# Kernel tuning notes

Hardware: AMD Instinct MI355X
Metric: run time of the kernel (lower is better)

## Reference

```python
import jax, jax.numpy as jnp
import numpy as np

N, IN_DIM, OUT_DIM = 8192, 256, 128
NEG_BIG = -9e15


def setup_inputs() -> dict:
    key = jax.random.key(0)
    k_x, k_a, k_w, k_att = jax.random.split(key, 4)
    X = jax.random.normal(k_x, (N, IN_DIM), dtype=jnp.float32)
    A = jax.random.randint(k_a, (N, N), 0, 2).astype(jnp.float32)
    # nn.Linear(in_dim, out_dim, bias=False): weight [out_dim, in_dim]
    W = jax.random.normal(k_w, (OUT_DIM, IN_DIM), dtype=jnp.float32) / np.sqrt(IN_DIM)
    # nn.Linear(out_dim, 1, bias=False): weight [1, out_dim] -> store as [out_dim]
    a_w = jax.random.normal(k_att, (OUT_DIM,), dtype=jnp.float32) / np.sqrt(OUT_DIM)
    return {"X": X, "A": A, "W": W, "a_w": a_w}


def reference(X, A, W, a_w):
    Wh = X @ W.T                                  # [N, out_dim]
    e = jax.nn.relu(Wh) @ a_w                      # [N]  (a(relu(Wh)).squeeze(-1))
    # NOTE: faithful to source: e broadcasts over rows -> score[i, j] = e[j]
    scores = jnp.where(A > 0, e[None, :], NEG_BIG)  # [N, N]
    attention = jax.nn.softmax(scores, axis=1)      # [N, N]
    h_prime = attention @ Wh                        # [N, out_dim]
    return jax.nn.relu(h_prime)
```

## Files before the change

### kernel.cpp

```cpp
#include <hip/hip_runtime.h>

typedef float        f32x4  __attribute__((ext_vector_type(4)));
typedef __bf16       bf16x8 __attribute__((ext_vector_type(8)));
typedef unsigned int u32x4  __attribute__((ext_vector_type(4)));

#define NN   8192
#define IND  256
#define OUTD 128
#define NB   144
#define KSPLIT 16
#define KRANGE 512
#define BT_BYTES (144 * 1024)

__device__ __forceinline__ bf16x8 cvt2(f32x4 a, f32x4 b) {
  bf16x8 r;
  r[0]=(__bf16)a[0]; r[1]=(__bf16)a[1]; r[2]=(__bf16)a[2]; r[3]=(__bf16)a[3];
  r[4]=(__bf16)b[0]; r[5]=(__bf16)b[1]; r[6]=(__bf16)b[2]; r[7]=(__bf16)b[3];
  return r;
}

__global__ __launch_bounds__(256) void k1_bt(const float* __restrict__ X,
                                             const float* __restrict__ W,
                                             const float* __restrict__ aw,
                                             __bf16* __restrict__ Bt) {
  __shared__ float red[4][16][128];
  const int tid  = threadIdx.x;
  const int lane = tid & 63;
  const int wave = tid >> 6;
  const int nlo  = lane & 15;
  const int quad = lane >> 4;
  const int rowBase = blockIdx.x * 16;

  const float* xp = X + (size_t)(rowBase + nlo) * IND + wave * 64 + quad * 8;
  f32x4 acc[8];
#pragma unroll
  for (int nt = 0; nt < 8; ++nt) acc[nt] = f32x4{0.f, 0.f, 0.f, 0.f};

#pragma unroll
  for (int kb = 0; kb < 64; kb += 32) {
    f32x4 a0 = *(const f32x4*)(xp + kb);
    f32x4 a1 = *(const f32x4*)(xp + kb + 4);
    bf16x8 af = cvt2(a0, a1);
#pragma unroll
    for (int nt = 0; nt < 8; ++nt) {
      const float* wp = W + (size_t)(nt * 16 + nlo) * IND + wave * 64 + kb + quad * 8;
      f32x4 b0 = *(const f32x4*)wp;
      f32x4 b1 = *(const f32x4*)(wp + 4);
      acc[nt] = __builtin_amdgcn_mfma_f32_16x16x32_bf16(af, cvt2(b0, b1), acc[nt], 0, 0, 0);
    }
  }
#pragma unroll
  for (int nt = 0; nt < 8; ++nt)
#pragma unroll
    for (int rg = 0; rg < 4; ++rg)
      red[wave][quad * 4 + rg][nt * 16 + nlo] = acc[nt][rg];
  __syncthreads();

  const int r  = tid >> 4;
  const int c0 = (tid & 15) * 8;
  f32x4 vlo = *(const f32x4*)&red[0][r][c0];
  f32x4 vhi = *(const f32x4*)&red[0][r][c0 + 4];
#pragma unroll
  for (int w = 1; w < 4; ++w) {
    vlo += *(const f32x4*)&red[w][r][c0];
    vhi += *(const f32x4*)&red[w][r][c0 + 4];
  }
  float pa = 0.f;
#pragma unroll
  for (int i = 0; i < 4; ++i) {
    pa += fmaxf(vlo[i], 0.f) * aw[c0 + i];
    pa += fmaxf(vhi[i], 0.f) * aw[c0 + 4 + i];
  }
#pragma unroll
  for (int off = 8; off; off >>= 1) pa += __shfl_xor(pa, off, 64);
  const float wexp = expf(pa);
  const int j = rowBase + r;

#pragma unroll
  for (int i = 0; i < 4; ++i)
    Bt[(size_t)(c0 + i) * NN + j] = (__bf16)(vlo[i] * wexp);
#pragma unroll
  for (int i = 0; i < 4; ++i)
    Bt[(size_t)(c0 + 4 + i) * NN + j] = (__bf16)(vhi[i] * wexp);
  if ((tid & 15) == 0)
    Bt[(size_t)OUTD * NN + j] = (__bf16)wexp;
  if (tid < 120) {
    const int row = 129 + (tid >> 3);
    const int cc  = rowBase + (tid & 7) * 2;
    Bt[(size_t)row * NN + cc]     = (__bf16)0.f;
    Bt[(size_t)row * NN + cc + 1] = (__bf16)0.f;
  }
}

__global__ __launch_bounds__(512) void k3_partial(const float* __restrict__ Adj,
                                                  const __bf16* __restrict__ Bt,
                                                  float* __restrict__ part) {
  extern __shared__ char btile[];
  const int tid  = threadIdx.x;
  const int lane = tid & 63;
  const int wv   = tid >> 6;
  const int nlo  = lane & 15;
  const int quad = lane >> 4;
  const int rowW = blockIdx.x * 128 + wv * 16;
  const int k0   = blockIdx.y * KRANGE;

  const float* ap = Adj + (size_t)(rowW + nlo) * NN + k0 + quad * 8;

  f32x4 aA[8], aB[8];
#pragma unroll
  for (int s4 = 0; s4 < 4; ++s4) {
    aA[2 * s4]     = __builtin_nontemporal_load((const f32x4*)(ap + s4 * 32));
    aA[2 * s4 + 1] = __builtin_nontemporal_load((const f32x4*)(ap + s4 * 32 + 4));
  }

#pragma unroll
  for (int it = 0; it < 18; ++it) {
    const int row = it * 8 + wv;
    const int swz = (row & 7) << 4;
    u32x4 v = *(const u32x4*)((const char*)(Bt + (size_t)row * NN + k0) + lane * 16);
    *(u32x4*)(btile + row * 1024 + ((lane * 16) ^ swz)) = v;
  }
  __syncthreads();

  f32x4 acc[9];
#pragma unroll
  for (int nt = 0; nt < 9; ++nt) acc[nt] = f32x4{0.f, 0.f, 0.f, 0.f};

  const int swzr = (nlo & 7) << 4;
  for (int c = 0; c < 4; ++c) {
    if (c < 3) {
      const int kc1 = (c + 1) * 128;
#pragma unroll
      for (int s4 = 0; s4 < 4; ++s4) {
        aB[2 * s4]     = __builtin_nontemporal_load((const f32x4*)(ap + kc1 + s4 * 32));
        aB[2 * s4 + 1] = __builtin_nontemporal_load((const f32x4*)(ap + kc1 + s4 * 32 + 4));
      }
    }
#pragma unroll
    for (int s4 = 0; s4 < 4; ++s4) {
      const int s = c * 4 + s4;
      bf16x8 af = cvt2(aA[2 * s4], aA[2 * s4 + 1]);
      const int cbl = s * 64 + quad * 16;
#pragma unroll
      for (int nt = 0; nt < 9; ++nt) {
        bf16x8 bf = *(const bf16x8*)(btile + (nt * 16 + nlo) * 1024 + (cbl ^ swzr));
        acc[nt] = __builtin_amdgcn_mfma_f32_16x16x32_bf16(af, bf, acc[nt], 0, 0, 0);
      }
    }
    if (c < 3) {
#pragma unroll
      for (int s = 0; s < 8; ++s) aA[s] = aB[s];
    }
  }

  float* pbase = part + ((size_t)blockIdx.y * NN + rowW) * NB;
#pragma unroll
  for (int nt = 0; nt < 8; ++nt)
#pragma unroll
    for (int rg = 0; rg < 4; ++rg)
      pbase[(size_t)(quad * 4 + rg) * NB + nt * 16 + nlo] = acc[nt][rg];
  if (nlo == 0) {
#pragma unroll
    for (int rg = 0; rg < 4; ++rg)
      pbase[(size_t)(quad * 4 + rg) * NB + 128] = acc[8][rg];
  }
}

__global__ __launch_bounds__(256) void k3_reduce(const float* __restrict__ part,
                                                 float* __restrict__ out) {
  const int col = threadIdx.x & 127;
  const int row = blockIdx.x * 2 + (threadIdx.x >> 7);
  float num = 0.f, den = 0.f;
#pragma unroll
  for (int s = 0; s < KSPLIT; ++s) {
    const size_t base = ((size_t)s * NN + row) * NB;
    num += part[base + col];
    den += part[base + 128];
  }
  out[(size_t)row * OUTD + col] = fmaxf(num / den, 0.f);
}

extern "C" void kernel_launch(void* const* d_in, const int* in_sizes, int n_in,
                              void* d_out, int out_size, void* d_ws, size_t ws_size,
                              hipStream_t stream) {
  const float* X  = (const float*)d_in[0];
  const float* A  = (const float*)d_in[1];
  const float* W  = (const float*)d_in[2];
  const float* aw = (const float*)d_in[3];
  float* out = (float*)d_out;

  char* ws = (char*)d_ws;
  __bf16* Bt   = (__bf16*)ws;
  float*  part = (float*)(ws + 4194304);

  static bool attr_done = false;
  if (!attr_done) {
    hipFuncSetAttribute((const void*)k3_partial,
                        hipFuncAttributeMaxDynamicSharedMemorySize, BT_BYTES);
    attr_done = true;
  }

  k1_bt<<<512, 256, 0, stream>>>(X, W, aw, Bt);
  k3_partial<<<dim3(64, KSPLIT), 512, BT_BYTES, stream>>>(A, Bt, part);
  k3_reduce<<<4096, 256, 0, stream>>>(part, out);
}
```

Baseline: 423.9 us.

## Stream Bt through small chunked LDS tiles to raise occupancy in k3_partial

The partial aggregation kernel used to stage a whole 144 KB Bt slice in dynamic LDS, which allowed only one 512-thread block per CU. It now loads Bt in 64-column chunks into a padded 20 KB static LDS tile, with a sync per chunk. It uses 256-thread blocks with a 4-block launch bound and halves KSPLIT to 8, giving 1024-wide K ranges. The aim is more resident waves to hide the latency of streaming the adjacency matrix. The cost is that the explicit A double-buffer prefetch is dropped, each chunk needs two barriers, and Bt is re-read from L2 by more row blocks.

```diff
diff --git a/kernel.cpp b/kernel.cpp
--- a/kernel.cpp
+++ b/kernel.cpp
@@ -2,15 +2,16 @@
 
 typedef float        f32x4  __attribute__((ext_vector_type(4)));
 typedef __bf16       bf16x8 __attribute__((ext_vector_type(8)));
-typedef unsigned int u32x4  __attribute__((ext_vector_type(4)));
+typedef unsigned int u32x2  __attribute__((ext_vector_type(2)));
 
 #define NN   8192
 #define IND  256
 #define OUTD 128
 #define NB   144
-#define KSPLIT 16
-#define KRANGE 512
-#define BT_BYTES (144 * 1024)
+#define KSPLIT 8
+#define KRANGE 1024
+#define KCHUNK 64
+#define BSTRIDE 72
 
 __device__ __forceinline__ bf16x8 cvt2(f32x4 a, f32x4 b) {
   bf16x8 r;
@@ -92,65 +93,55 @@
   }
 }
 
-__global__ __launch_bounds__(512) void k3_partial(const float* __restrict__ Adj,
-                                                  const __bf16* __restrict__ Bt,
-                                                  float* __restrict__ part) {
-  extern __shared__ char btile[];
+__global__ __launch_bounds__(256, 4) void k3_partial(const float* __restrict__ Adj,
+                                                     const __bf16* __restrict__ Bt,
+                                                     float* __restrict__ part) {
+  __shared__ unsigned short bt[NB * BSTRIDE];
   const int tid  = threadIdx.x;
   const int lane = tid & 63;
-  const int wv   = tid >> 6;
+  const int wave = tid >> 6;
   const int nlo  = lane & 15;
   const int quad = lane >> 4;
-  const int rowW = blockIdx.x * 128 + wv * 16;
+  const int rowW = blockIdx.x * 64 + wave * 16;
   const int k0   = blockIdx.y * KRANGE;
 
-  const float* ap = Adj + (size_t)(rowW + nlo) * NN + k0 + quad * 8;
-
-  f32x4 aA[8], aB[8];
-#pragma unroll
-  for (int s4 = 0; s4 < 4; ++s4) {
-    aA[2 * s4]     = __builtin_nontemporal_load((const f32x4*)(ap + s4 * 32));
-    aA[2 * s4 + 1] = __builtin_nontemporal_load((const f32x4*)(ap + s4 * 32 + 4));
-  }
-
-#pragma unroll
-  for (int it = 0; it < 18; ++it) {
-    const int row = it * 8 + wv;
-    const int swz = (row & 7) << 4;
-    u32x4 v = *(const u32x4*)((const char*)(Bt + (size_t)row * NN + k0) + lane * 16);
-    *(u32x4*)(btile + row * 1024 + ((lane * 16) ^ swz)) = v;
-  }
-  __syncthreads();
+  const int brow = tid >> 4;
+  const int bcol = (tid & 15) * 4;
 
   f32x4 acc[9];
 #pragma unroll
   for (int nt = 0; nt < 9; ++nt) acc[nt] = f32x4{0.f, 0.f, 0.f, 0.f};
 
-  const int swzr = (nlo & 7) << 4;
-  for (int c = 0; c < 4; ++c) {
-    if (c < 3) {
-      const int kc1 = (c + 1) * 128;
+  const float*  ap = Adj + (size_t)(rowW + nlo) * NN + quad * 8 + k0;
+  const __bf16* bq = Bt + (size_t)brow * NN + k0 + bcol;
+
+  for (int c = 0; c < KRANGE / KCHUNK; ++c) {
+    const int kc = c * KCHUNK;
+    u32x2 breg[9];
 #pragma unroll
-      for (int s4 = 0; s4 < 4; ++s4) {
-        aB[2 * s4]     = __builtin_nontemporal_load((const f32x4*)(ap + kc1 + s4 * 32));
-        aB[2 * s4 + 1] = __builtin_nontemporal_load((const f32x4*)(ap + kc1 + s4 * 32 + 4));
-      }
+    for (int rr = 0; rr < 9; ++rr)
+      breg[rr] = *(const u32x2*)(bq + (size_t)(rr * 16) * NN + kc);
+    f32x4 areg[4];
+#pragma unroll
+    for (int s = 0; s < 2; ++s) {
+      areg[2 * s]     = __builtin_nontemporal_load((const f32x4*)(ap + kc + s * 32));
+      areg[2 * s + 1] = __builtin_nontemporal_load((const f32x4*)(ap + kc + s * 32 + 4));
     }
 #pragma unroll
-    for (int s4 = 0; s4 < 4; ++s4) {
-      const int s = c * 4 + s4;
-      bf16x8 af = cvt2(aA[2 * s4], aA[2 * s4 + 1]);
-      const int cbl = s * 64 + quad * 16;
+    for (int rr = 0; rr < 9; ++rr)
+      *(u32x2*)(bt + (rr * 16 + brow) * BSTRIDE + bcol) = breg[rr];
+    __syncthreads();
+#pragma unroll
+    for (int s = 0; s < 2; ++s) {
+      bf16x8 af = cvt2(areg[2 * s], areg[2 * s + 1]);
+      const unsigned short* bp = bt + s * 32 + quad * 8;
 #pragma unroll
       for (int nt = 0; nt < 9; ++nt) {
-        bf16x8 bf = *(const bf16x8*)(btile + (nt * 16 + nlo) * 1024 + (cbl ^ swzr));
+        bf16x8 bf = *(const bf16x8*)(bp + (nt * 16 + nlo) * BSTRIDE);
         acc[nt] = __builtin_amdgcn_mfma_f32_16x16x32_bf16(af, bf, acc[nt], 0, 0, 0);
       }
     }
-    if (c < 3) {
-#pragma unroll
-      for (int s = 0; s < 8; ++s) aA[s] = aB[s];
-    }
+    __syncthreads();
   }
 
   float* pbase = part + ((size_t)blockIdx.y * NN + rowW) * NB;
@@ -193,14 +184,7 @@
   __bf16* Bt   = (__bf16*)ws;
   float*  part = (float*)(ws + 4194304);
 
-  static bool attr_done = false;
-  if (!attr_done) {
-    hipFuncSetAttribute((const void*)k3_partial,
-                        hipFuncAttributeMaxDynamicSharedMemorySize, BT_BYTES);
-    attr_done = true;
-  }
-
   k1_bt<<<512, 256, 0, stream>>>(X, W, aw, Bt);
-  k3_partial<<<dim3(64, KSPLIT), 512, BT_BYTES, stream>>>(A, Bt, part);
+  k3_partial<<<dim3(128, KSPLIT), 256, 0, stream>>>(A, Bt, part);
   k3_reduce<<<4096, 256, 0, stream>>>(part, out);
 }
```

Result: no change. 420.3 us (-0.9%).
